# Kernel tuning notes

Measured on AMD Instinct MI355X. Metric: run time of the kernel, lower is better.

The kernel has to match this reference:

```python
import jax, jax.numpy as jnp
import numpy as np

B, S, D, NH = 4, 2048, 512, 8
HD = D // NH
SCALING = HD ** -0.5


def setup_inputs() -> dict:
    key = jax.random.key(0)
    ks = jax.random.split(key, 8)
    w_std = (2.0 / (D + D)) ** 0.5  # xavier_uniform-ish scale
    inp = {
        "query": jax.random.normal(ks[0], (B, S, D), jnp.float32),
        "key": jax.random.normal(ks[1], (B, S, D), jnp.float32),
        "value": jax.random.normal(ks[2], (B, S, D), jnp.float32),
        "key_mask": jnp.ones((B, S), dtype=bool),
        "attn_mask": jnp.tril(jnp.ones((S, S), dtype=bool)),  # causal, per docstring
        "Wq": jax.random.normal(ks[3], (D, D), jnp.float32) * w_std,
        "bq": jnp.zeros((D,), jnp.float32),
        "Wk": jax.random.normal(ks[4], (D, D), jnp.float32) * w_std,
        "bk": jnp.zeros((D,), jnp.float32),
        "Wv": jax.random.normal(ks[5], (D, D), jnp.float32) * w_std,
        "bv": jnp.zeros((D,), jnp.float32),
        "Wo": jax.random.normal(ks[6], (D, D), jnp.float32) * w_std,
        "bo": jnp.zeros((D,), jnp.float32),
    }
    return inp


def reference(query, key, value, key_mask, attn_mask, Wq, bq, Wk, bk, Wv, bv, Wo, bo):
    b, q_len, d = query.shape
    k_len = key.shape[1]
    # projections (nn.Linear: x @ W.T + b)
    q = (query @ Wq.T + bq) * SCALING
    k = key @ Wk.T + bk
    v = value @ Wv.T + bv
    q = q.reshape(b, q_len, NH, HD)
    k = k.reshape(b, k_len, NH, HD)
    v = v.reshape(b, k_len, NH, HD)
    # scores: [b, q, k, n]
    attn = jnp.einsum('bqnh,bknh->bqkn', q, k)
    # key_mask: 1 = attend; masked_fill(~mask, -inf)
    attn = jnp.where(key_mask[:, None, :, None], attn, -jnp.inf)
    # attn_mask: [q, k], 1 = attend
    attn = jnp.where(attn_mask[None, :, :, None], attn, -jnp.inf)
    attn = jax.nn.softmax(attn, axis=2)
    # dropout p=0.0 in eval -> identity
    out = jnp.einsum('bqkn,bknh->bqnh', attn, v)
    out = out.reshape(b, q_len, d)
    out = out @ Wo.T + bo
    return (out, attn)
```

## Files before the change

### kernel.cpp

```cpp
#include <hip/hip_runtime.h>


typedef short bf8 __attribute__((ext_vector_type(8)));
typedef short bf4 __attribute__((ext_vector_type(4)));
typedef float f4  __attribute__((ext_vector_type(4)));

#define MFMA16(a, b, c) __builtin_amdgcn_mfma_f32_16x16x32_bf16(a, b, c, 0, 0, 0)

static __device__ __forceinline__ short f2bf(float x) {
  unsigned u = __builtin_bit_cast(unsigned, x);
  unsigned r = (u + 0x7fffu + ((u >> 16) & 1u)) >> 16;
  return (short)r;
}
static __device__ __forceinline__ f4 zero4() { f4 z = {0.f, 0.f, 0.f, 0.f}; return z; }

__global__ __launch_bounds__(256, 3) void gemm_qkv(const float* __restrict__ Aq,
                                                   const float* __restrict__ Ak,
                                                   const float* __restrict__ Av,
                                                   const float* __restrict__ Wq,
                                                   const float* __restrict__ Wk,
                                                   const float* __restrict__ Wv,
                                                   const float* __restrict__ bq,
                                                   const float* __restrict__ bk,
                                                   const float* __restrict__ bv,
                                                   short* __restrict__ Qo,
                                                   short* __restrict__ Ko,
                                                   short* __restrict__ Vo) {
  __shared__ short As[128 * 40];
  __shared__ short Bs[128 * 40];
  const int z = blockIdx.z;
  const float* A = (z == 0) ? Aq : (z == 1) ? Ak : Av;
  const float* W = (z == 0) ? Wq : (z == 1) ? Wk : Wv;
  const float* bias = (z == 0) ? bq : (z == 1) ? bk : bv;
  short* out = (z == 0) ? Qo : (z == 1) ? Ko : Vo;
  const float scale = (z == 0) ? 0.125f : 1.0f;

  const int tid = threadIdx.x;
  const int wave = tid >> 6, lane = tid & 63, quad = lane >> 4, col = lane & 15;
  const int m0 = blockIdx.y * 128, n0 = blockIdx.x * 128;
  const int row_off = (wave >> 1) * 64, col_off = (wave & 1) * 64;

  f4 acc[4][4];
#pragma unroll
  for (int i = 0; i < 4; ++i)
#pragma unroll
    for (int j = 0; j < 4; ++j) acc[i][j] = zero4();

  float bvv[4];
#pragma unroll
  for (int nt = 0; nt < 4; ++nt) bvv[nt] = bias[n0 + col_off + nt * 16 + col];

  for (int k0 = 0; k0 < 512; k0 += 32) {
#pragma unroll
    for (int i = 0; i < 4; ++i) {
      int c = i * 256 + tid;
      int r = c >> 3, cc = (c & 7) * 4;
      f4 v = *(const f4*)(A + (size_t)(m0 + r) * 512 + k0 + cc);
      bf4 s = {f2bf(v[0]), f2bf(v[1]), f2bf(v[2]), f2bf(v[3])};
      *(bf4*)&As[r * 40 + cc] = s;
      f4 w = *(const f4*)(W + (size_t)(n0 + r) * 512 + k0 + cc);
      bf4 sw = {f2bf(w[0]), f2bf(w[1]), f2bf(w[2]), f2bf(w[3])};
      *(bf4*)&Bs[r * 40 + cc] = sw;
    }
    __syncthreads();
    bf8 af[4], bw[4];
#pragma unroll
    for (int mt = 0; mt < 4; ++mt) af[mt] = *(const bf8*)&As[(row_off + mt * 16 + col) * 40 + quad * 8];
#pragma unroll
    for (int nt = 0; nt < 4; ++nt) bw[nt] = *(const bf8*)&Bs[(col_off + nt * 16 + col) * 40 + quad * 8];
#pragma unroll
    for (int mt = 0; mt < 4; ++mt)
#pragma unroll
      for (int nt = 0; nt < 4; ++nt) acc[mt][nt] = MFMA16(af[mt], bw[nt], acc[mt][nt]);
    __syncthreads();
  }

  __shared__ short Ct[128 * 136];
  if (z != 2) {
#pragma unroll
    for (int mt = 0; mt < 4; ++mt)
#pragma unroll
      for (int nt = 0; nt < 4; ++nt)
#pragma unroll
        for (int r = 0; r < 4; ++r)
          Ct[(row_off + mt * 16 + quad * 4 + r) * 136 + col_off + nt * 16 + col] =
              f2bf((acc[mt][nt][r] + bvv[nt]) * scale);
  } else {
#pragma unroll
    for (int mt = 0; mt < 4; ++mt)
#pragma unroll
      for (int nt = 0; nt < 4; ++nt) {
        bf4 s = {f2bf(acc[mt][nt][0] + bvv[nt]), f2bf(acc[mt][nt][1] + bvv[nt]),
                 f2bf(acc[mt][nt][2] + bvv[nt]), f2bf(acc[mt][nt][3] + bvv[nt])};
        *(bf4*)&Ct[(col_off + nt * 16 + col) * 136 + row_off + mt * 16 + quad * 4] = s;
      }
  }
  __syncthreads();
#pragma unroll
  for (int it = 0; it < 8; ++it) {
    int c = it * 256 + tid;
    if (z != 2) {
      int row = c >> 4, ch = (c & 15) * 8;
      int m = m0 + row, bb = m >> 11, sidx = m & 2047;
      int cg = n0 + ch, n = cg >> 6, h = cg & 63;
      bf8 v = *(const bf8*)&Ct[row * 136 + ch];
      *(bf8*)(out + ((size_t)((bb * 8 + n) * 2048 + sidx)) * 64 + h) = v;
    } else {
      int j = c >> 4, sc8 = (c & 15) * 8;
      int cg = n0 + j, n = cg >> 6, h = cg & 63;
      int m = m0 + sc8, bb = m >> 11, srow = m & 2047;
      bf8 v = *(const bf8*)&Ct[j * 136 + sc8];
      *(bf8*)(out + ((size_t)((bb * 8 + n) * 64 + h)) * 2048 + srow) = v;
    }
  }
}

__global__ __launch_bounds__(256, 2) void gemm_out(const short* __restrict__ A,
                                                   const float* __restrict__ W,
                                                   const float* __restrict__ bias,
                                                   float* __restrict__ out) {
  __shared__ short As[128 * 40];
  __shared__ short Bs[128 * 40];
  const int tid = threadIdx.x;
  const int wave = tid >> 6, lane = tid & 63, quad = lane >> 4, col = lane & 15;
  const int m0 = blockIdx.y * 128, n0 = blockIdx.x * 128;
  const int row_off = (wave >> 1) * 64, col_off = (wave & 1) * 64;

  f4 acc[4][4];
#pragma unroll
  for (int i = 0; i < 4; ++i)
#pragma unroll
    for (int j = 0; j < 4; ++j) acc[i][j] = zero4();

  float bv[4];
#pragma unroll
  for (int nt = 0; nt < 4; ++nt) bv[nt] = bias[n0 + col_off + nt * 16 + col];

  for (int k0 = 0; k0 < 512; k0 += 32) {
#pragma unroll
    for (int i = 0; i < 4; ++i) {
      int c = i * 256 + tid;
      int r = c >> 3, cc = (c & 7) * 4;
      *(bf4*)&As[r * 40 + cc] = *(const bf4*)(A + (size_t)(m0 + r) * 512 + k0 + cc);
      f4 w = *(const f4*)(W + (size_t)(n0 + r) * 512 + k0 + cc);
      bf4 sw = {f2bf(w[0]), f2bf(w[1]), f2bf(w[2]), f2bf(w[3])};
      *(bf4*)&Bs[r * 40 + cc] = sw;
    }
    __syncthreads();
    bf8 af[4], bw[4];
#pragma unroll
    for (int mt = 0; mt < 4; ++mt) af[mt] = *(const bf8*)&As[(row_off + mt * 16 + col) * 40 + quad * 8];
#pragma unroll
    for (int nt = 0; nt < 4; ++nt) bw[nt] = *(const bf8*)&Bs[(col_off + nt * 16 + col) * 40 + quad * 8];
#pragma unroll
    for (int mt = 0; mt < 4; ++mt)
#pragma unroll
      for (int nt = 0; nt < 4; ++nt) acc[mt][nt] = MFMA16(af[mt], bw[nt], acc[mt][nt]);
    __syncthreads();
  }

#pragma unroll
  for (int mt = 0; mt < 4; ++mt)
#pragma unroll
    for (int nt = 0; nt < 4; ++nt) {
      int rb = m0 + row_off + mt * 16 + quad * 4;
      int cg = n0 + col_off + nt * 16 + col;
#pragma unroll
      for (int r = 0; r < 4; ++r) out[(size_t)(rb + r) * 512 + cg] = acc[mt][nt][r] + bv[nt];
    }
}

#define SLAB 1092

__global__ __launch_bounds__(512, 4) void attn_k(const short* __restrict__ Q,
                                                 const short* __restrict__ K,
                                                 const short* __restrict__ Vt,
                                                 short* __restrict__ O,
                                                 float* __restrict__ attn) {
  __shared__ float Pl[8 * SLAB];
  __shared__ float rl_s[128];
  const int tid = threadIdx.x;
  const int wv = tid >> 6, lane = tid & 63, quad = lane >> 4, col = lane & 15;
  const int bid = blockIdx.x;
  const int b = bid & 3;
  const int q0 = (127 - (bid >> 2)) * 16;
  const int q_hi = q0 + 15;
  const int nsteps = (q_hi >> 6) + 1;

  const size_t hb = (size_t)(b * 8 + wv) * 2048;
  const bf8 aq0 = *(const bf8*)(Q + (hb + q0 + col) * 64 + quad * 8);
  const bf8 aq1 = *(const bf8*)(Q + (hb + q0 + col) * 64 + 32 + quad * 8);

  float rl[4] = {0.f, 0.f, 0.f, 0.f};
  for (int ks = 0; ks < nsteps; ++ks) {
    int k0 = ks << 6;
#pragma unroll
    for (int kt = 0; kt < 4; ++kt) {
      int kb = k0 + kt * 16;
      if (kb <= q_hi) {
        const short* kp = K + (hb + kb + col) * 64 + quad * 8;
        bf8 b0 = *(const bf8*)kp;
        bf8 b1 = *(const bf8*)(kp + 32);
        f4 sc = zero4();
        sc = MFMA16(aq0, b0, sc);
        sc = MFMA16(aq1, b1, sc);
        if (kb + 15 <= q0) {
#pragma unroll
          for (int r = 0; r < 4; ++r) rl[r] += __expf(sc[r]);
        } else {
          int kg = kb + col;
#pragma unroll
          for (int r = 0; r < 4; ++r) rl[r] += (kg <= q0 + quad * 4 + r) ? __expf(sc[r]) : 0.f;
        }
      }
    }
  }
#pragma unroll
  for (int r = 0; r < 4; ++r) {
    float v = rl[r];
    v += __shfl_xor(v, 1);
    v += __shfl_xor(v, 2);
    v += __shfl_xor(v, 4);
    v += __shfl_xor(v, 8);
    rl[r] = 1.0f / v;
  }
  if (col == 0) {
#pragma unroll
    for (int r = 0; r < 4; ++r) rl_s[wv * 16 + quad * 4 + r] = rl[r];
  }
  __syncthreads();

  const int gq = tid >> 5, gc0 = tid & 31;
  const int gnb = (gc0 & 1) * 4, gk0 = gc0 >> 1;
  float rl8[4];
#pragma unroll
  for (int j = 0; j < 4; ++j) rl8[j] = rl_s[(gnb + j) * 16 + gq];

  f4 oacc[4];
#pragma unroll
  for (int t = 0; t < 4; ++t) oacc[t] = zero4();

  for (int ks = 0; ks < nsteps; ++ks) {
    int k0 = ks << 6;
#pragma unroll
    for (int kt = 0; kt < 4; ++kt) {
      int kb = k0 + kt * 16;
      f4 p = zero4();
      if (kb <= q_hi) {
        const short* kp = K + (hb + kb + col) * 64 + quad * 8;
        bf8 b0 = *(const bf8*)kp;
        bf8 b1 = *(const bf8*)(kp + 32);
        f4 sc = zero4();
        sc = MFMA16(aq0, b0, sc);
        sc = MFMA16(aq1, b1, sc);
        if (kb + 15 <= q0) {
#pragma unroll
          for (int r = 0; r < 4; ++r) p[r] = __expf(sc[r]);
        } else {
          int kg = kb + col;
#pragma unroll
          for (int r = 0; r < 4; ++r) p[r] = (kg <= q0 + quad * 4 + r) ? __expf(sc[r]) : 0.f;
        }
      }
      float* wp = Pl + wv * SLAB + (quad * 4) * 68 + kt * 16 + col;
#pragma unroll
      for (int r = 0; r < 4; ++r) wp[r * 68] = p[r];
    }
    __syncthreads();
    {
      float* dst = attn + ((size_t)(b * 2048 + q0 + gq) * 2048 + k0) * 8;
      const float* base = Pl + gq * 68;
#pragma unroll
      for (int i = 0; i < 4; ++i) {
        int k = gk0 + 16 * i;
        f4 v;
#pragma unroll
        for (int j = 0; j < 4; ++j) v[j] = base[(gnb + j) * SLAB + k] * rl8[j];
        __builtin_nontemporal_store(v, (f4*)(dst + k * 8 + gnb));
      }
    }
#pragma unroll
    for (int kk = 0; kk < 2; ++kk) {
      const float* pp = Pl + wv * SLAB + col * 68 + kk * 32 + quad * 8;
      f4 a0 = *(const f4*)pp;
      f4 a1 = *(const f4*)(pp + 4);
      bf8 ap = {f2bf(a0[0]), f2bf(a0[1]), f2bf(a0[2]), f2bf(a0[3]),
                f2bf(a1[0]), f2bf(a1[1]), f2bf(a1[2]), f2bf(a1[3])};
#pragma unroll
      for (int t = 0; t < 4; ++t) {
        const short* vp = Vt + ((size_t)((b * 8 + wv) * 64 + t * 16 + col)) * 2048 + k0 + kk * 32 + quad * 8;
        bf8 bvv = *(const bf8*)vp;
        oacc[t] = MFMA16(ap, bvv, oacc[t]);
      }
    }
    __syncthreads();
  }

  int klim = nsteps << 6;
  if (klim < 2048) {
    int nf4 = (2048 - klim) * 2;
#pragma unroll 1
    for (int qq = 0; qq < 16; ++qq) {
      f4* dst = (f4*)(attn + ((size_t)(b * 2048 + q0 + qq) * 2048 + klim) * 8);
      for (int i = tid; i < nf4; i += 512) __builtin_nontemporal_store(zero4(), dst + i);
    }
  }

#pragma unroll
  for (int t = 0; t < 4; ++t)
#pragma unroll
    for (int r = 0; r < 4; ++r)
      Pl[(quad * 4 + r) * 516 + wv * 64 + t * 16 + col] = oacc[t][r] * rl[r];
  __syncthreads();
  {
    const float* src = Pl + gq * 516;
    short* dst = O + (size_t)(b * 2048 + q0 + gq) * 512;
#pragma unroll
    for (int i = 0; i < 4; ++i) {
      int cc = (gc0 + 32 * i) * 4;
      f4 v = *(const f4*)(src + cc);
      bf4 s = {f2bf(v[0]), f2bf(v[1]), f2bf(v[2]), f2bf(v[3])};
      *(bf4*)(dst + cc) = s;
    }
  }
}

extern "C" void kernel_launch(void* const* d_in, const int* in_sizes, int n_in,
                              void* d_out, int out_size, void* d_ws, size_t ws_size,
                              hipStream_t stream) {
  const float* query = (const float*)d_in[0];
  const float* key = (const float*)d_in[1];
  const float* value = (const float*)d_in[2];
  const float* Wq = (const float*)d_in[5];
  const float* bq = (const float*)d_in[6];
  const float* Wk = (const float*)d_in[7];
  const float* bk = (const float*)d_in[8];
  const float* Wv = (const float*)d_in[9];
  const float* bv = (const float*)d_in[10];
  const float* Wo = (const float*)d_in[11];
  const float* bo = (const float*)d_in[12];

  char* ws = (char*)d_ws;
  const size_t MB8 = (size_t)8 * 1024 * 1024;
  short* Qb = (short*)(ws);
  short* Kb = (short*)(ws + MB8);
  short* Vt = (short*)(ws + 2 * MB8);
  short* Ob = (short*)(ws + 3 * MB8);

  float* out = (float*)d_out;
  float* attn = out + (size_t)4 * 2048 * 512;

  gemm_qkv<<<dim3(4, 64, 3), 256, 0, stream>>>(query, key, value, Wq, Wk, Wv, bq, bk, bv, Qb, Kb, Vt);
  attn_k<<<512, 512, 0, stream>>>(Qb, Kb, Vt, Ob, attn);
  gemm_out<<<dim3(4, 64), 256, 0, stream>>>(Ob, Wo, bo, out);
}
```

Before: 834.5 us.

## Double-buffer attention P tile, batch K/V loads, and move zero-fill first

The attention kernel now ping-pongs between two shared-memory P buffers, which removes the second barrier in each key step. K fragments for all four subtiles and V fragments are loaded in a batch before the MFMAs so the loads can overlap. The zero-fill of the masked upper attention region moves to kernel start, and the QKV GEMM overlays its staging and output shared tiles with a union. Doubling Pl raises the attention kernel's LDS use, which may lower occupancy, and the extra fragment registers add register pressure.

```diff
diff --git a/kernel.cpp b/kernel.cpp
--- a/kernel.cpp
+++ b/kernel.cpp
@@ -13,6 +13,11 @@
   return (short)r;
 }
 static __device__ __forceinline__ f4 zero4() { f4 z = {0.f, 0.f, 0.f, 0.f}; return z; }
+
+union SmemQKV {
+  struct { short As[128 * 40]; short Bs[128 * 40]; } st;
+  short Ct[128 * 136];
+};
 
 __global__ __launch_bounds__(256, 3) void gemm_qkv(const float* __restrict__ Aq,
                                                    const float* __restrict__ Ak,
@@ -26,8 +31,7 @@
                                                    short* __restrict__ Qo,
                                                    short* __restrict__ Ko,
                                                    short* __restrict__ Vo) {
-  __shared__ short As[128 * 40];
-  __shared__ short Bs[128 * 40];
+  __shared__ SmemQKV u;
   const int z = blockIdx.z;
   const float* A = (z == 0) ? Aq : (z == 1) ? Ak : Av;
   const float* W = (z == 0) ? Wq : (z == 1) ? Wk : Wv;
@@ -57,17 +61,17 @@
       int r = c >> 3, cc = (c & 7) * 4;
       f4 v = *(const f4*)(A + (size_t)(m0 + r) * 512 + k0 + cc);
       bf4 s = {f2bf(v[0]), f2bf(v[1]), f2bf(v[2]), f2bf(v[3])};
-      *(bf4*)&As[r * 40 + cc] = s;
+      *(bf4*)&u.st.As[r * 40 + cc] = s;
       f4 w = *(const f4*)(W + (size_t)(n0 + r) * 512 + k0 + cc);
       bf4 sw = {f2bf(w[0]), f2bf(w[1]), f2bf(w[2]), f2bf(w[3])};
-      *(bf4*)&Bs[r * 40 + cc] = sw;
+      *(bf4*)&u.st.Bs[r * 40 + cc] = sw;
     }
     __syncthreads();
     bf8 af[4], bw[4];
 #pragma unroll
-    for (int mt = 0; mt < 4; ++mt) af[mt] = *(const bf8*)&As[(row_off + mt * 16 + col) * 40 + quad * 8];
-#pragma unroll
-    for (int nt = 0; nt < 4; ++nt) bw[nt] = *(const bf8*)&Bs[(col_off + nt * 16 + col) * 40 + quad * 8];
+    for (int mt = 0; mt < 4; ++mt) af[mt] = *(const bf8*)&u.st.As[(row_off + mt * 16 + col) * 40 + quad * 8];
+#pragma unroll
+    for (int nt = 0; nt < 4; ++nt) bw[nt] = *(const bf8*)&u.st.Bs[(col_off + nt * 16 + col) * 40 + quad * 8];
 #pragma unroll
     for (int mt = 0; mt < 4; ++mt)
 #pragma unroll
@@ -75,7 +79,6 @@
     __syncthreads();
   }
 
-  __shared__ short Ct[128 * 136];
   if (z != 2) {
 #pragma unroll
     for (int mt = 0; mt < 4; ++mt)
@@ -83,7 +86,7 @@
       for (int nt = 0; nt < 4; ++nt)
 #pragma unroll
         for (int r = 0; r < 4; ++r)
-          Ct[(row_off + mt * 16 + quad * 4 + r) * 136 + col_off + nt * 16 + col] =
+          u.Ct[(row_off + mt * 16 + quad * 4 + r) * 136 + col_off + nt * 16 + col] =
               f2bf((acc[mt][nt][r] + bvv[nt]) * scale);
   } else {
 #pragma unroll
@@ -92,7 +95,7 @@
       for (int nt = 0; nt < 4; ++nt) {
         bf4 s = {f2bf(acc[mt][nt][0] + bvv[nt]), f2bf(acc[mt][nt][1] + bvv[nt]),
                  f2bf(acc[mt][nt][2] + bvv[nt]), f2bf(acc[mt][nt][3] + bvv[nt])};
-        *(bf4*)&Ct[(col_off + nt * 16 + col) * 136 + row_off + mt * 16 + quad * 4] = s;
+        *(bf4*)&u.Ct[(col_off + nt * 16 + col) * 136 + row_off + mt * 16 + quad * 4] = s;
       }
   }
   __syncthreads();
@@ -103,13 +106,13 @@
       int row = c >> 4, ch = (c & 15) * 8;
       int m = m0 + row, bb = m >> 11, sidx = m & 2047;
       int cg = n0 + ch, n = cg >> 6, h = cg & 63;
-      bf8 v = *(const bf8*)&Ct[row * 136 + ch];
+      bf8 v = *(const bf8*)&u.Ct[row * 136 + ch];
       *(bf8*)(out + ((size_t)((bb * 8 + n) * 2048 + sidx)) * 64 + h) = v;
     } else {
       int j = c >> 4, sc8 = (c & 15) * 8;
       int cg = n0 + j, n = cg >> 6, h = cg & 63;
       int m = m0 + sc8, bb = m >> 11, srow = m & 2047;
-      bf8 v = *(const bf8*)&Ct[j * 136 + sc8];
+      bf8 v = *(const bf8*)&u.Ct[j * 136 + sc8];
       *(bf8*)(out + ((size_t)((bb * 8 + n) * 64 + h)) * 2048 + srow) = v;
     }
   }
@@ -171,13 +174,14 @@
 }
 
 #define SLAB 1092
+#define PBUF (8 * SLAB)
 
 __global__ __launch_bounds__(512, 4) void attn_k(const short* __restrict__ Q,
                                                  const short* __restrict__ K,
                                                  const short* __restrict__ Vt,
                                                  short* __restrict__ O,
                                                  float* __restrict__ attn) {
-  __shared__ float Pl[8 * SLAB];
+  __shared__ float Pl[2 * PBUF];
   __shared__ float rl_s[128];
   const int tid = threadIdx.x;
   const int wv = tid >> 6, lane = tid & 63, quad = lane >> 4, col = lane & 15;
@@ -187,6 +191,16 @@
   const int q_hi = q0 + 15;
   const int nsteps = (q_hi >> 6) + 1;
 
+  const int klim = nsteps << 6;
+  if (klim < 2048) {
+    int nf4 = (2048 - klim) * 2;
+#pragma unroll 1
+    for (int qq = 0; qq < 16; ++qq) {
+      f4* dst = (f4*)(attn + ((size_t)(b * 2048 + q0 + qq) * 2048 + klim) * 8);
+      for (int i = tid; i < nf4; i += 512) __builtin_nontemporal_store(zero4(), dst + i);
+    }
+  }
+
   const size_t hb = (size_t)(b * 8 + wv) * 2048;
   const bf8 aq0 = *(const bf8*)(Q + (hb + q0 + col) * 64 + quad * 8);
   const bf8 aq1 = *(const bf8*)(Q + (hb + q0 + col) * 64 + 32 + quad * 8);
@@ -194,16 +208,23 @@
   float rl[4] = {0.f, 0.f, 0.f, 0.f};
   for (int ks = 0; ks < nsteps; ++ks) {
     int k0 = ks << 6;
+    bf8 kf0[4], kf1[4];
 #pragma unroll
     for (int kt = 0; kt < 4; ++kt) {
       int kb = k0 + kt * 16;
       if (kb <= q_hi) {
         const short* kp = K + (hb + kb + col) * 64 + quad * 8;
-        bf8 b0 = *(const bf8*)kp;
-        bf8 b1 = *(const bf8*)(kp + 32);
+        kf0[kt] = *(const bf8*)kp;
+        kf1[kt] = *(const bf8*)(kp + 32);
+      }
+    }
+#pragma unroll
+    for (int kt = 0; kt < 4; ++kt) {
+      int kb = k0 + kt * 16;
+      if (kb <= q_hi) {
         f4 sc = zero4();
-        sc = MFMA16(aq0, b0, sc);
-        sc = MFMA16(aq1, b1, sc);
+        sc = MFMA16(aq0, kf0[kt], sc);
+        sc = MFMA16(aq1, kf1[kt], sc);
         if (kb + 15 <= q0) {
 #pragma unroll
           for (int r = 0; r < 4; ++r) rl[r] += __expf(sc[r]);
@@ -242,17 +263,25 @@
 
   for (int ks = 0; ks < nsteps; ++ks) {
     int k0 = ks << 6;
+    float* buf = Pl + (ks & 1) * PBUF;
+    bf8 kf0[4], kf1[4];
+#pragma unroll
+    for (int kt = 0; kt < 4; ++kt) {
+      int kb = k0 + kt * 16;
+      if (kb <= q_hi) {
+        const short* kp = K + (hb + kb + col) * 64 + quad * 8;
+        kf0[kt] = *(const bf8*)kp;
+        kf1[kt] = *(const bf8*)(kp + 32);
+      }
+    }
 #pragma unroll
     for (int kt = 0; kt < 4; ++kt) {
       int kb = k0 + kt * 16;
       f4 p = zero4();
       if (kb <= q_hi) {
-        const short* kp = K + (hb + kb + col) * 64 + quad * 8;
-        bf8 b0 = *(const bf8*)kp;
-        bf8 b1 = *(const bf8*)(kp + 32);
         f4 sc = zero4();
-        sc = MFMA16(aq0, b0, sc);
-        sc = MFMA16(aq1, b1, sc);
+        sc = MFMA16(aq0, kf0[kt], sc);
+        sc = MFMA16(aq1, kf1[kt], sc);
         if (kb + 15 <= q0) {
 #pragma unroll
           for (int r = 0; r < 4; ++r) p[r] = __expf(sc[r]);
@@ -262,14 +291,23 @@
           for (int r = 0; r < 4; ++r) p[r] = (kg <= q0 + quad * 4 + r) ? __expf(sc[r]) : 0.f;
         }
       }
-      float* wp = Pl + wv * SLAB + (quad * 4) * 68 + kt * 16 + col;
+      float* wp = buf + wv * SLAB + (quad * 4) * 68 + kt * 16 + col;
 #pragma unroll
       for (int r = 0; r < 4; ++r) wp[r * 68] = p[r];
     }
     __syncthreads();
+
+    bf8 vr[8];
+#pragma unroll
+    for (int kk = 0; kk < 2; ++kk)
+#pragma unroll
+      for (int t = 0; t < 4; ++t)
+        vr[kk * 4 + t] =
+            *(const bf8*)(Vt + ((size_t)((b * 8 + wv) * 64 + t * 16 + col)) * 2048 + k0 + kk * 32 + quad * 8);
+
     {
       float* dst = attn + ((size_t)(b * 2048 + q0 + gq) * 2048 + k0) * 8;
-      const float* base = Pl + gq * 68;
+      const float* base = Pl + (ks & 1) * PBUF + gq * 68;
 #pragma unroll
       for (int i = 0; i < 4; ++i) {
         int k = gk0 + 16 * i;
@@ -281,31 +319,17 @@
     }
 #pragma unroll
     for (int kk = 0; kk < 2; ++kk) {
-      const float* pp = Pl + wv * SLAB + col * 68 + kk * 32 + quad * 8;
+      const float* pp = buf + wv * SLAB + col * 68 + kk * 32 + quad * 8;
       f4 a0 = *(const f4*)pp;
       f4 a1 = *(const f4*)(pp + 4);
       bf8 ap = {f2bf(a0[0]), f2bf(a0[1]), f2bf(a0[2]), f2bf(a0[3]),
                 f2bf(a1[0]), f2bf(a1[1]), f2bf(a1[2]), f2bf(a1[3])};
 #pragma unroll
-      for (int t = 0; t < 4; ++t) {
-        const short* vp = Vt + ((size_t)((b * 8 + wv) * 64 + t * 16 + col)) * 2048 + k0 + kk * 32 + quad * 8;
-        bf8 bvv = *(const bf8*)vp;
-        oacc[t] = MFMA16(ap, bvv, oacc[t]);
-      }
-    }
-    __syncthreads();
-  }
-
-  int klim = nsteps << 6;
-  if (klim < 2048) {
-    int nf4 = (2048 - klim) * 2;
-#pragma unroll 1
-    for (int qq = 0; qq < 16; ++qq) {
-      f4* dst = (f4*)(attn + ((size_t)(b * 2048 + q0 + qq) * 2048 + klim) * 8);
-      for (int i = tid; i < nf4; i += 512) __builtin_nontemporal_store(zero4(), dst + i);
-    }
-  }
-
+      for (int t = 0; t < 4; ++t) oacc[t] = MFMA16(ap, vr[kk * 4 + t], oacc[t]);
+    }
+  }
+
+  __syncthreads();
 #pragma unroll
   for (int t = 0; t < 4; ++t)
 #pragma unroll
```

Result: slower. 851.4 us (+2.0%).
